# Kernel tuning notes

Measured on AMD Instinct MI355X. Metric: run time of the kernel, lower is better.

The kernel has to match this reference:

```python
import jax, jax.numpy as jnp
import numpy as np

GRID = 64
K = 5          # splat loop extent in original
FX = FY = 120.0
U0 = V0 = 36.0
TZ = 2.5

# gaussianBlock(sigma=0.2, k=10) but only indices [0:5,0:5] are read -> center at 5
_II, _JJ = np.meshgrid(np.arange(K), np.arange(K), indexing='ij')
_GK = jnp.asarray(np.exp(-np.sqrt((_II - 5.0) ** 2 + (_JJ - 5.0) ** 2) / (2.0 * 0.2)).astype(np.float32))


def _eul2rot(t):
    s0, s1, s2 = jnp.sin(t[0]), jnp.sin(t[1]), jnp.sin(t[2])
    c0, c1, c2 = jnp.cos(t[0]), jnp.cos(t[1]), jnp.cos(t[2])
    return jnp.array([
        [c1 * c2, s0 * s1 * c2 - s2 * c0, s1 * c0 * c2 + s0 * s2],
        [s2 * c1, s0 * s1 * s2 + c0 * c2, s1 * s2 * c0 - s0 * c2],
        [-s1, s0 * c1, c0 * c1],
    ])


def _project_images(pc, R):
    """pc: [B,N,3] -> normalized splat images [B, GRID*GRID]."""
    cam = jnp.einsum('ij,bnj->bni', R, pc)          # R @ x
    z = cam[..., 2] + TZ                             # translation only in z
    u = FX * cam[..., 0] / z + U0
    v = FY * cam[..., 1] / z + V0
    x4 = jnp.round(u).astype(jnp.int32)              # round-half-even, same as python round
    y4 = jnp.round(v).astype(jnp.int32)
    ptv = (x4 >= 0) & (x4 <= GRID) & (y4 >= 0) & (y4 <= GRID)
    off = jnp.arange(K, dtype=jnp.int32) + K // 2    # i + k//2 in 2..6
    px = x4[:, :, None, None] - off[None, None, :, None]   # [B,N,K,1]
    py = y4[:, :, None, None] - off[None, None, None, :]   # [B,N,1,K]
    valid = ptv[:, :, None, None] & (px >= 0) & (px <= GRID) & (py >= 0) & (py <= GRID)
    # note: px,py <= 62 whenever ptv holds, so indices never exceed 63
    flat = jnp.where(valid, px * GRID + py, 0)       # [B,N,K,K]
    vals = jnp.where(valid, _GK[None, None], 0.0)    # [B,N,K,K]
    B = pc.shape[0]
    img = jax.vmap(lambda f, w: jnp.zeros(GRID * GRID, jnp.float32).at[f].add(w))(
        flat.reshape(B, -1), vals.reshape(B, -1))
    return img / jnp.max(img, axis=-1, keepdims=True)


def _bce_sum(inp, tgt):
    # torch BCELoss(reduction='sum') with log clamped at -100
    lp = jnp.maximum(jnp.log(inp), -100.0)
    lq = jnp.maximum(jnp.log(1.0 - inp), -100.0)
    return -jnp.sum(tgt * lp + (1.0 - tgt) * lq)


def setup_inputs() -> dict:
    key = jax.random.key(0)
    k1, k2, k3 = jax.random.split(key, 3)
    pc1 = 0.25 * jax.random.normal(k1, (16, 30000, 3), dtype=jnp.float32)
    pc2 = 0.25 * jax.random.normal(k2, (16, 30000, 3), dtype=jnp.float32)
    rotations = 2.0 * jnp.pi * jax.random.uniform(k3, (2, 3), dtype=jnp.float32)
    return {'pc1_batch': pc1, 'pc2_batch': pc2, 'rotations': rotations}


def reference(pc1_batch, pc2_batch, rotations):
    loss = jnp.float32(0.0)
    for r in range(2):  # fixed small set of rotations
        R = _eul2rot(rotations[r])
        e1 = _project_images(pc1_batch, R)
        e2 = _project_images(pc2_batch, R)
        loss = loss + _bce_sum(e1, e2)
    return loss
```

## Files before the change

### kernel.cpp

```cpp
#include <hip/hip_runtime.h>
#include <math.h>

#define NPTS    30000
#define NB      16
#define CNT_W   65
#define CNT_SZ  (65 * 65)
#define NIMG    64
#define IMG_SZ  4096
#define NSPLIT  4
#define GPS     (NPTS / 4 / NSPLIT)

__device__ inline void eul2rot(const float* t, float R[9]) {
    float s0 = sinf(t[0]), s1 = sinf(t[1]), s2 = sinf(t[2]);
    float c0 = cosf(t[0]), c1 = cosf(t[1]), c2 = cosf(t[2]);
    R[0] = c1 * c2; R[1] = s0 * s1 * c2 - s2 * c0; R[2] = s1 * c0 * c2 + s0 * s2;
    R[3] = s2 * c1; R[4] = s0 * s1 * s2 + c0 * c2; R[5] = s1 * s2 * c0 - s0 * c2;
    R[6] = -s1;     R[7] = s0 * c1;                R[8] = c0 * c1;
}

__device__ inline void splat1(float x, float y, float zz, const float R[9],
                              unsigned* lcnt) {
    float cx = R[0] * x + R[1] * y + R[2] * zz;
    float cy = R[3] * x + R[4] * y + R[5] * zz;
    float cz = R[6] * x + R[7] * y + R[8] * zz;
    float z  = cz + 2.5f;
    float u  = 120.0f * cx / z + 36.0f;
    float v  = 120.0f * cy / z + 36.0f;
    int x4 = (int)rintf(u);
    int y4 = (int)rintf(v);
    if (x4 >= 0 && x4 <= 64 && y4 >= 0 && y4 <= 64)
        atomicAdd(&lcnt[x4 * CNT_W + y4], 1u);
}

__global__ __launch_bounds__(512) void hist_kernel(const float* __restrict__ pc1,
                                                   const float* __restrict__ pc2,
                                                   const float* __restrict__ rot,
                                                   unsigned* __restrict__ pcnts,
                                                   float* __restrict__ out) {
    __shared__ unsigned lcnt[CNT_SZ];
    int bid   = blockIdx.x;
    int split = bid & (NSPLIT - 1);
    int imgi  = bid >> 2;
    int b = imgi & 15;
    int c = (imgi >> 4) & 1;
    int r = imgi >> 5;
    int tid = threadIdx.x;

    if (bid == 0 && tid == 0) out[0] = 0.0f;

    for (int i = tid; i < CNT_SZ; i += 512) lcnt[i] = 0u;

    float R[9];
    eul2rot(rot + 3 * r, R);
    const float* pc = (c ? pc2 : pc1) + (size_t)b * NPTS * 3;
    const float4* pc4 = (const float4*)pc;
    __syncthreads();

    int gend = (split + 1) * GPS;
    for (int g = split * GPS + tid; g < gend; g += 512) {
        float4 a = pc4[3 * g + 0];
        float4 bq = pc4[3 * g + 1];
        float4 cq = pc4[3 * g + 2];
        splat1(a.x, a.y, a.z, R, lcnt);
        splat1(a.w, bq.x, bq.y, R, lcnt);
        splat1(bq.z, bq.w, cq.x, R, lcnt);
        splat1(cq.y, cq.z, cq.w, R, lcnt);
    }
    __syncthreads();

    unsigned* g = pcnts + (size_t)bid * CNT_SZ;
    for (int i = tid; i < CNT_SZ; i += 512) g[i] = lcnt[i];
}

__global__ __launch_bounds__(1024) void convbce_kernel(const unsigned* __restrict__ pcnts,
                                                       float* __restrict__ out) {
    __shared__ float lcA[CNT_SZ];
    __shared__ float lcB[CNT_SZ];
    __shared__ float redA[16], redB[16], redS[16];
    int bid = blockIdx.x;
    int b = bid & 15, r = bid >> 4;
    int i1 = r * 32 + b;
    int i2 = r * 32 + 16 + b;
    int tid = threadIdx.x;

    const unsigned* pa = pcnts + (size_t)i1 * NSPLIT * CNT_SZ;
    const unsigned* pb = pcnts + (size_t)i2 * NSPLIT * CNT_SZ;
    for (int i = tid; i < CNT_SZ; i += 1024) {
        lcA[i] = (float)(pa[i] + pa[i + CNT_SZ] + pa[i + 2 * CNT_SZ] + pa[i + 3 * CNT_SZ]);
        lcB[i] = (float)(pb[i] + pb[i + CNT_SZ] + pb[i + 2 * CNT_SZ] + pb[i + 3 * CNT_SZ]);
    }

    float GK[25];
#pragma unroll
    for (int i = 0; i < 5; i++)
#pragma unroll
        for (int j = 0; j < 5; j++) {
            float d = sqrtf((float)((i - 5) * (i - 5) + (j - 5) * (j - 5)));
            GK[i * 5 + j] = expf(-d / 0.4f);
        }
    __syncthreads();

    float cA[4], cB[4];
    float mA = 0.0f, mB = 0.0f;
#pragma unroll
    for (int k = 0; k < 4; k++) {
        int o = tid + k * 1024;
        int px = o >> 6, py = o & 63;
        float sA = 0.0f, sB = 0.0f;
#pragma unroll
        for (int i = 0; i < 5; i++) {
            int x = px + 2 + i;
            if (x > 64) continue;
            const float* rowA = &lcA[x * CNT_W];
            const float* rowB = &lcB[x * CNT_W];
#pragma unroll
            for (int j = 0; j < 5; j++) {
                int y = py + 2 + j;
                if (y > 64) continue;
                float w = GK[i * 5 + j];
                sA += w * rowA[y];
                sB += w * rowB[y];
            }
        }
        cA[k] = sA; cB[k] = sB;
        mA = fmaxf(mA, sA); mB = fmaxf(mB, sB);
    }

#pragma unroll
    for (int off = 32; off > 0; off >>= 1) {
        mA = fmaxf(mA, __shfl_down(mA, off));
        mB = fmaxf(mB, __shfl_down(mB, off));
    }
    int wave = tid >> 6;
    if ((tid & 63) == 0) { redA[wave] = mA; redB[wave] = mB; }
    __syncthreads();
    float maxA = redA[0], maxB = redB[0];
#pragma unroll
    for (int w = 1; w < 16; w++) {
        maxA = fmaxf(maxA, redA[w]);
        maxB = fmaxf(maxB, redB[w]);
    }

    float invA = 1.0f / maxA, invB = 1.0f / maxB;
    float s = 0.0f;
#pragma unroll
    for (int k = 0; k < 4; k++) {
        float e1 = cA[k] * invA;
        float e2 = cB[k] * invB;
        float lp = fmaxf(logf(e1), -100.0f);
        float lq = fmaxf(logf(1.0f - e1), -100.0f);
        s += e2 * lp + (1.0f - e2) * lq;
    }
#pragma unroll
    for (int off = 32; off > 0; off >>= 1) s += __shfl_down(s, off);
    if ((tid & 63) == 0) redS[wave] = s;
    __syncthreads();
    if (tid == 0) {
        float tot = 0.0f;
#pragma unroll
        for (int w = 0; w < 16; w++) tot += redS[w];
        atomicAdd(out, -tot);
    }
}

extern "C" void kernel_launch(void* const* d_in, const int* in_sizes, int n_in,
                              void* d_out, int out_size, void* d_ws, size_t ws_size,
                              hipStream_t stream) {
    const float* pc1 = (const float*)d_in[0];
    const float* pc2 = (const float*)d_in[1];
    const float* rot = (const float*)d_in[2];
    float* out = (float*)d_out;

    unsigned* pcnts = (unsigned*)d_ws;

    hist_kernel<<<NIMG * NSPLIT, 512, 0, stream>>>(pc1, pc2, rot, pcnts, out);
    convbce_kernel<<<32, 1024, 0, stream>>>(pcnts, out);
}
```

Before: 22.40 us.

## Splat both rotations per point load and use fast reciprocal projection

```diff
diff --git a/kernel.cpp b/kernel.cpp
--- a/kernel.cpp
+++ b/kernel.cpp
@@ -6,7 +6,6 @@
 #define CNT_W   65
 #define CNT_SZ  (65 * 65)
 #define NIMG    64
-#define IMG_SZ  4096
 #define NSPLIT  4
 #define GPS     (NPTS / 4 / NSPLIT)
 
@@ -23,9 +22,9 @@
     float cx = R[0] * x + R[1] * y + R[2] * zz;
     float cy = R[3] * x + R[4] * y + R[5] * zz;
     float cz = R[6] * x + R[7] * y + R[8] * zz;
-    float z  = cz + 2.5f;
-    float u  = 120.0f * cx / z + 36.0f;
-    float v  = 120.0f * cy / z + 36.0f;
+    float inv = __builtin_amdgcn_rcpf(cz + 2.5f);
+    float u = fmaf(120.0f * cx, inv, 36.0f);
+    float v = fmaf(120.0f * cy, inv, 36.0f);
     int x4 = (int)rintf(u);
     int y4 = (int)rintf(v);
     if (x4 >= 0 && x4 <= 64 && y4 >= 0 && y4 <= 64)
@@ -37,39 +36,41 @@
                                                    const float* __restrict__ rot,
                                                    unsigned* __restrict__ pcnts,
                                                    float* __restrict__ out) {
-    __shared__ unsigned lcnt[CNT_SZ];
+    __shared__ unsigned lc0[CNT_SZ];
+    __shared__ unsigned lc1[CNT_SZ];
     int bid   = blockIdx.x;
     int split = bid & (NSPLIT - 1);
-    int imgi  = bid >> 2;
-    int b = imgi & 15;
-    int c = (imgi >> 4) & 1;
-    int r = imgi >> 5;
+    int cb    = bid >> 2;
+    int b = cb & 15;
+    int c = cb >> 4;
     int tid = threadIdx.x;
 
     if (bid == 0 && tid == 0) out[0] = 0.0f;
 
-    for (int i = tid; i < CNT_SZ; i += 512) lcnt[i] = 0u;
+    for (int i = tid; i < CNT_SZ; i += 512) { lc0[i] = 0u; lc1[i] = 0u; }
 
-    float R[9];
-    eul2rot(rot + 3 * r, R);
+    float R0[9], R1[9];
+    eul2rot(rot, R0);
+    eul2rot(rot + 3, R1);
     const float* pc = (c ? pc2 : pc1) + (size_t)b * NPTS * 3;
     const float4* pc4 = (const float4*)pc;
     __syncthreads();
 
     int gend = (split + 1) * GPS;
     for (int g = split * GPS + tid; g < gend; g += 512) {
-        float4 a = pc4[3 * g + 0];
+        float4 a  = pc4[3 * g + 0];
         float4 bq = pc4[3 * g + 1];
         float4 cq = pc4[3 * g + 2];
-        splat1(a.x, a.y, a.z, R, lcnt);
-        splat1(a.w, bq.x, bq.y, R, lcnt);
-        splat1(bq.z, bq.w, cq.x, R, lcnt);
-        splat1(cq.y, cq.z, cq.w, R, lcnt);
+        splat1(a.x, a.y, a.z, R0, lc0);   splat1(a.x, a.y, a.z, R1, lc1);
+        splat1(a.w, bq.x, bq.y, R0, lc0); splat1(a.w, bq.x, bq.y, R1, lc1);
+        splat1(bq.z, bq.w, cq.x, R0, lc0);splat1(bq.z, bq.w, cq.x, R1, lc1);
+        splat1(cq.y, cq.z, cq.w, R0, lc0);splat1(cq.y, cq.z, cq.w, R1, lc1);
     }
     __syncthreads();
 
-    unsigned* g = pcnts + (size_t)bid * CNT_SZ;
-    for (int i = tid; i < CNT_SZ; i += 512) g[i] = lcnt[i];
+    unsigned* g0 = pcnts + (size_t)((c * 16 + b) * NSPLIT + split) * CNT_SZ;
+    unsigned* g1 = pcnts + (size_t)((32 + c * 16 + b) * NSPLIT + split) * CNT_SZ;
+    for (int i = tid; i < CNT_SZ; i += 512) { g0[i] = lc0[i]; g1[i] = lc1[i]; }
 }
 
 __global__ __launch_bounds__(1024) void convbce_kernel(const unsigned* __restrict__ pcnts,
@@ -173,6 +174,6 @@
 
     unsigned* pcnts = (unsigned*)d_ws;
 
-    hist_kernel<<<NIMG * NSPLIT, 512, 0, stream>>>(pc1, pc2, rot, pcnts, out);
+    hist_kernel<<<2 * NB * NSPLIT, 512, 0, stream>>>(pc1, pc2, rot, pcnts, out);
     convbce_kernel<<<32, 1024, 0, stream>>>(pcnts, out);
 }
```

Measured after the change: 23.29 us. +4.0%, slower.
